# Optimization experiments

Measured on AMD Instinct MI355X. Metric: run time of the kernel, lower is better.

The kernel has to match this reference:

```python
import jax, jax.numpy as jnp
import numpy as np

N_NODES = 100000
N_EDGES = 1600000
IN_F = 512
OUT_F = 128


def setup_inputs() -> dict:
    key = jax.random.key(0)
    k1, k2, k3, k4, k5 = jax.random.split(key, 5)
    features = jax.random.normal(k1, (N_NODES, IN_F), dtype=jnp.float32)
    # xavier_uniform-like init for the [in, out] weight
    limit = float(np.sqrt(6.0 / (IN_F + OUT_F)))
    weight = jax.random.uniform(k2, (IN_F, OUT_F), dtype=jnp.float32, minval=-limit, maxval=limit)
    edge_src = jax.random.randint(k3, (N_EDGES,), 0, N_NODES, dtype=jnp.int32)
    edge_dst = jax.random.randint(k4, (N_EDGES,), 0, N_NODES, dtype=jnp.int32)
    edge_w = jax.random.uniform(k5, (N_EDGES,), dtype=jnp.float32)
    return {"features": features, "weight": weight, "edge_src": edge_src,
            "edge_dst": edge_dst, "edge_w": edge_w}


def reference(features, weight, edge_src, edge_dst, edge_w):
    # support = features @ W  (dense GEMM, [N, out])
    support = features @ weight
    # spmm(adj, support): adj in COO form -> gather source rows, scale by
    # edge weight, scatter-add into destination rows.
    msgs = support[edge_src] * edge_w[:, None]            # [E, out]
    out = jax.ops.segment_sum(msgs, edge_dst, num_segments=N_NODES)  # [N, out]
    return jax.nn.relu(out)
```

## Files before the change

### kernel.cpp

```cpp
#include <hip/hip_runtime.h>
#include <hip/hip_bf16.h>

#define M_N 100000
#define K_F 512
#define N_F 128
#define N_E 1600000
#define NBUK 782
#define CAP 2560
#define EPB 8192

typedef __attribute__((ext_vector_type(8))) short bf16x8;
typedef __attribute__((ext_vector_type(4))) float f32x4;

__device__ __forceinline__ unsigned short f2bf(float f) {
  unsigned u = __float_as_uint(f);
  u += 0x7FFFu + ((u >> 16) & 1u);
  return (unsigned short)(u >> 16);
}

__device__ __forceinline__ unsigned pkbf(float a, float b) {
  __hip_bfloat162 h = __float22bfloat162_rn(make_float2(a, b));
  return *(unsigned*)&h;
}

__global__ void k_wt(const float* __restrict__ w, unsigned short* __restrict__ wtb,
                     int* __restrict__ gcur) {
  int idx = blockIdx.x * 256 + threadIdx.x;
  if (idx < NBUK) gcur[idx] = idx * CAP;
  int k = idx >> 7, n = idx & 127;
  wtb[n * K_F + k] = f2bf(w[idx]);
}

__global__ __launch_bounds__(256, 2) void k_gemm(const float* __restrict__ A,
                       const unsigned short* __restrict__ Bt,
                       unsigned short* __restrict__ S) {
  __shared__ __align__(16) float As[3][128 * 32];
  __shared__ __align__(16) unsigned short Bs[3][128 * 32];
  const int tid = threadIdx.x;
  const int lane = tid & 63;
  const int wv = tid >> 6;
  const int lr = lane & 15, lq = lane >> 4;
  const int bm0 = blockIdx.x * 128;
  const int wrow = wv * 32;

  f32x4 acc[2][8] = {};

#define STAGE(T, BUF)                                                          \
  do {                                                                         \
    _Pragma("unroll") for (int i = 0; i < 4; i++) {                            \
      int idx = i * 256 + tid;                                                 \
      int r = idx >> 3, c = idx & 7;                                           \
      int gr = bm0 + r; if (gr > M_N - 1) gr = M_N - 1;                        \
      const float* srcp = A + (size_t)gr * K_F + (T) * 32 + (c ^ (r & 7)) * 4; \
      __builtin_amdgcn_global_load_lds(                                        \
          (const __attribute__((address_space(1))) void*)srcp,                 \
          (__attribute__((address_space(3))) void*)&As[BUF][(i * 256 + wv * 64) * 4], \
          16, 0, 0);                                                           \
    }                                                                          \
    _Pragma("unroll") for (int i = 0; i < 2; i++) {                            \
      int idx = i * 256 + tid;                                                 \
      int n = idx >> 2, c = idx & 3;                                           \
      const unsigned short* srcb = Bt + (size_t)n * K_F + (T) * 32 + (c ^ (n & 3)) * 8; \
      __builtin_amdgcn_global_load_lds(                                        \
          (const __attribute__((address_space(1))) void*)srcb,                 \
          (__attribute__((address_space(3))) void*)&Bs[BUF][(i * 256 + wv * 64) * 8], \
          16, 0, 0);                                                           \
    }                                                                          \
  } while (0)

  STAGE(0, 0);
  STAGE(1, 1);

#pragma unroll
  for (int t = 0; t < 16; t++) {
    if (t < 15) asm volatile("s_waitcnt vmcnt(6)" ::: "memory");
    else        asm volatile("s_waitcnt vmcnt(0)" ::: "memory");
    __builtin_amdgcn_sched_barrier(0);
    __builtin_amdgcn_s_barrier();
    __builtin_amdgcn_sched_barrier(0);
    if (t < 14) {
      switch ((t + 2) % 3) {
        case 0: STAGE(t + 2, 0); break;
        case 1: STAGE(t + 2, 1); break;
        default: STAGE(t + 2, 2); break;
      }
    }
    const int cb_ = t % 3;
    bf16x8 pb[8];
#pragma unroll
    for (int n = 0; n < 8; n++) {
      int r = n * 16 + lr;
      int cc = lq ^ (r & 3);
      pb[n] = *(const bf16x8*)&Bs[cb_][r * 32 + cc * 8];
    }
#pragma unroll
    for (int m = 0; m < 2; m++) {
      int R = wrow + m * 16 + lr;
      int cb = lq * 2, sw = R & 7;
      f32x4 f0 = *(const f32x4*)&As[cb_][R * 32 + ((cb) ^ sw) * 4];
      f32x4 f1 = *(const f32x4*)&As[cb_][R * 32 + ((cb + 1) ^ sw) * 4];
      uint4 u;
      u.x = pkbf(f0[0], f0[1]);
      u.y = pkbf(f0[2], f0[3]);
      u.z = pkbf(f1[0], f1[1]);
      u.w = pkbf(f1[2], f1[3]);
      bf16x8 af = *(bf16x8*)&u;
#pragma unroll
      for (int n = 0; n < 8; n++)
        acc[m][n] = __builtin_amdgcn_mfma_f32_16x16x32_bf16(af, pb[n], acc[m][n], 0, 0, 0);
    }
  }
#undef STAGE

#pragma unroll
  for (int m = 0; m < 2; m++)
#pragma unroll
    for (int j = 0; j < 4; j++) {
      int gr = bm0 + wrow + m * 16 + lq * 4 + j;
      if (gr < M_N) {
#pragma unroll
        for (int n = 0; n < 8; n++)
          S[(size_t)gr * N_F + n * 16 + lr] = f2bf(acc[m][n][j]);
      }
    }
}

__global__ __launch_bounds__(512) void k_bin(const int* __restrict__ src,
                                             const int* __restrict__ dst,
                                             const float* __restrict__ w,
                                             int* __restrict__ gcur,
                                             uint2* __restrict__ ebin) {
  __shared__ int lh[NBUK];
  __shared__ int lb[NBUK];
  const int tid = threadIdx.x;
  const int e0 = blockIdx.x * EPB;
  for (int b = tid; b < NBUK; b += 512) lh[b] = 0;
  __syncthreads();
#pragma unroll
  for (int i = 0; i < EPB / 512; i++) {
    int e = e0 + i * 512 + tid;
    if (e < N_E) atomicAdd(&lh[dst[e] >> 7], 1);
  }
  __syncthreads();
  for (int b = tid; b < NBUK; b += 512) {
    int c = lh[b];
    lb[b] = c ? atomicAdd(&gcur[b], c) : 0;
    lh[b] = 0;
  }
  __syncthreads();
#pragma unroll
  for (int i = 0; i < EPB / 512; i++) {
    int e = e0 + i * 512 + tid;
    if (e < N_E) {
      int d = dst[e];
      int bk = d >> 7;
      int rank = atomicAdd(&lh[bk], 1);
      ebin[lb[bk] + rank] =
          make_uint2(((unsigned)(d & 127) << 17) | (unsigned)src[e],
                     __float_as_uint(w[e]));
    }
  }
}

__device__ __forceinline__ void fma8(float* acc, float wgt, uint4 v) {
  acc[0] = fmaf(wgt, __uint_as_float(v.x << 16), acc[0]);
  acc[1] = fmaf(wgt, __uint_as_float(v.x & 0xFFFF0000u), acc[1]);
  acc[2] = fmaf(wgt, __uint_as_float(v.y << 16), acc[2]);
  acc[3] = fmaf(wgt, __uint_as_float(v.y & 0xFFFF0000u), acc[3]);
  acc[4] = fmaf(wgt, __uint_as_float(v.z << 16), acc[4]);
  acc[5] = fmaf(wgt, __uint_as_float(v.z & 0xFFFF0000u), acc[5]);
  acc[6] = fmaf(wgt, __uint_as_float(v.w << 16), acc[6]);
  acc[7] = fmaf(wgt, __uint_as_float(v.w & 0xFFFF0000u), acc[7]);
}

__global__ __launch_bounds__(512) void k_bspmm(const unsigned short* __restrict__ S,
                                               const int* __restrict__ gcur,
                                               const uint2* __restrict__ ebin,
                                               float* __restrict__ out) {
  __shared__ uint2 srt[CAP];
  __shared__ int hist[128], excl[129], cur[128];
  const int b = blockIdx.x;
  const int t = threadIdx.x;
  const int cnt = gcur[b] - b * CAP;
  const uint2* eb = ebin + (size_t)b * CAP;

  if (t < 128) hist[t] = 0;
  __syncthreads();

  uint2 er[5];
  int have = 0;
#pragma unroll
  for (int j = 0; j < 5; j++) {
    int i = j * 512 + t;
    if (i < cnt) { er[j] = eb[i]; have = j + 1; }
  }
#pragma unroll
  for (int j = 0; j < 5; j++)
    if (j < have) atomicAdd(&hist[(er[j].x >> 17) & 127], 1);
  __syncthreads();

  if (t < 128) excl[t + 1] = hist[t];
  if (t == 0) excl[0] = 0;
  __syncthreads();
  for (int off = 1; off < 128; off <<= 1) {
    int v = 0;
    if (t < 128) {
      v = excl[t + 1];
      if (t + 1 > off) v += excl[t + 1 - off];
    }
    __syncthreads();
    if (t < 128) excl[t + 1] = v;
    __syncthreads();
  }
  if (t < 128) cur[t] = excl[t];
  __syncthreads();

#pragma unroll
  for (int j = 0; j < 5; j++)
    if (j < have) {
      int dl = (er[j].x >> 17) & 127;
      int r = atomicAdd(&cur[dl], 1);
      srt[r] = er[j];
    }
  __syncthreads();

  const int lane = t & 63, wv = t >> 6;
  const int g = lane >> 4;
  const int l = lane & 15;
  for (int nn = 0; nn < 16; nn++) {
    const int ln = wv * 16 + nn;
    const int s = excl[ln], e = excl[ln + 1];
    float acc[8] = {0.f, 0.f, 0.f, 0.f, 0.f, 0.f, 0.f, 0.f};
    int i = s + g;
    for (; i + 4 < e; i += 8) {
      uint2 p0 = srt[i];
      uint2 p1 = srt[i + 4];
      uint4 v0 = *(const uint4*)(S + (size_t)(p0.x & 0x1FFFFu) * N_F + l * 8);
      uint4 v1 = *(const uint4*)(S + (size_t)(p1.x & 0x1FFFFu) * N_F + l * 8);
      fma8(acc, __uint_as_float(p0.y), v0);
      fma8(acc, __uint_as_float(p1.y), v1);
    }
    if (i < e) {
      uint2 p = srt[i];
      uint4 v = *(const uint4*)(S + (size_t)(p.x & 0x1FFFFu) * N_F + l * 8);
      fma8(acc, __uint_as_float(p.y), v);
    }
#pragma unroll
    for (int j = 0; j < 8; j++) {
      acc[j] += __shfl_xor(acc[j], 16, 64);
      acc[j] += __shfl_xor(acc[j], 32, 64);
      acc[j] = fmaxf(acc[j], 0.f);
    }
    const int node = b * 128 + ln;
    if (g < 2 && node < M_N) {
      float4 r = make_float4(acc[g * 4 + 0], acc[g * 4 + 1],
                             acc[g * 4 + 2], acc[g * 4 + 3]);
      *(float4*)(out + (size_t)node * N_F + l * 8 + g * 4) = r;
    }
  }
}

extern "C" void kernel_launch(void* const* d_in, const int* in_sizes, int n_in,
                              void* d_out, int out_size, void* d_ws, size_t ws_size,
                              hipStream_t stream) {
  const float* features = (const float*)d_in[0];
  const float* weight   = (const float*)d_in[1];
  const int* edge_src   = (const int*)d_in[2];
  const int* edge_dst   = (const int*)d_in[3];
  const float* edge_w   = (const float*)d_in[4];
  float* out = (float*)d_out;

  char* ws = (char*)d_ws;
  size_t off = 0;
  unsigned short* support = (unsigned short*)(ws + off); off += (size_t)M_N * N_F * 2;
  unsigned short* wtb     = (unsigned short*)(ws + off); off += (size_t)N_F * K_F * 2;
  int* gcur   = (int*)(ws + off); off += 4096;
  uint2* ebin = (uint2*)(ws + off); off += ((size_t)NBUK * CAP + 64) * 8;

  k_wt<<<256, 256, 0, stream>>>(weight, wtb, gcur);
  k_gemm<<<(M_N + 127) / 128, 256, 0, stream>>>(features, wtb, support);
  k_bin<<<(N_E + EPB - 1) / EPB, 512, 0, stream>>>(edge_src, edge_dst, edge_w, gcur, ebin);
  k_bspmm<<<NBUK, 512, 0, stream>>>(support, gcur, ebin, out);
}
```

Baseline: 170.2 us.

## Merge GEMM and edge-binning kernels into one launch with block-role split

Folds the edge binning kernel into the GEMM kernel: the first 782 blocks compute the dense GEMM tile and the remaining blocks perform the per-bucket histogram and scatter of edges, reusing the GEMM's shared memory for the histograms. This is meant to overlap the memory-bound binning with the GEMM and remove one kernel launch and its tail. In exchange, binning blocks now run with 256 threads instead of 512 and inherit the GEMM's large shared-memory footprint and launch bounds, which may limit their occupancy.

```diff
diff --git a/kernel.cpp b/kernel.cpp
--- a/kernel.cpp
+++ b/kernel.cpp
@@ -8,6 +8,8 @@
 #define NBUK 782
 #define CAP 2560
 #define EPB 8192
+#define NGEMM 782
+#define NBIN ((N_E + EPB - 1) / EPB)
 
 typedef __attribute__((ext_vector_type(8))) short bf16x8;
 typedef __attribute__((ext_vector_type(4))) float f32x4;
@@ -31,19 +33,24 @@
   wtb[n * K_F + k] = f2bf(w[idx]);
 }
 
-__global__ __launch_bounds__(256, 2) void k_gemm(const float* __restrict__ A,
+__global__ __launch_bounds__(256, 2) void k_fused(const float* __restrict__ A,
                        const unsigned short* __restrict__ Bt,
-                       unsigned short* __restrict__ S) {
+                       unsigned short* __restrict__ S,
+                       const int* __restrict__ esrc, const int* __restrict__ edst,
+                       const float* __restrict__ ew,
+                       int* __restrict__ gcur, uint2* __restrict__ ebin) {
   __shared__ __align__(16) float As[3][128 * 32];
   __shared__ __align__(16) unsigned short Bs[3][128 * 32];
   const int tid = threadIdx.x;
-  const int lane = tid & 63;
-  const int wv = tid >> 6;
-  const int lr = lane & 15, lq = lane >> 4;
-  const int bm0 = blockIdx.x * 128;
-  const int wrow = wv * 32;
-
-  f32x4 acc[2][8] = {};
+
+  if (blockIdx.x < NGEMM) {
+    const int lane = tid & 63;
+    const int wv = tid >> 6;
+    const int lr = lane & 15, lq = lane >> 4;
+    const int bm0 = blockIdx.x * 128;
+    const int wrow = wv * 32;
+
+    f32x4 acc[2][8] = {};
 
 #define STAGE(T, BUF)                                                          \
   do {                                                                         \
@@ -68,96 +75,90 @@
     }                                                                          \
   } while (0)
 
-  STAGE(0, 0);
-  STAGE(1, 1);
-
-#pragma unroll
-  for (int t = 0; t < 16; t++) {
-    if (t < 15) asm volatile("s_waitcnt vmcnt(6)" ::: "memory");
-    else        asm volatile("s_waitcnt vmcnt(0)" ::: "memory");
-    __builtin_amdgcn_sched_barrier(0);
-    __builtin_amdgcn_s_barrier();
-    __builtin_amdgcn_sched_barrier(0);
-    if (t < 14) {
-      switch ((t + 2) % 3) {
-        case 0: STAGE(t + 2, 0); break;
-        case 1: STAGE(t + 2, 1); break;
-        default: STAGE(t + 2, 2); break;
-      }
-    }
-    const int cb_ = t % 3;
-    bf16x8 pb[8];
-#pragma unroll
-    for (int n = 0; n < 8; n++) {
-      int r = n * 16 + lr;
-      int cc = lq ^ (r & 3);
-      pb[n] = *(const bf16x8*)&Bs[cb_][r * 32 + cc * 8];
-    }
-#pragma unroll
-    for (int m = 0; m < 2; m++) {
-      int R = wrow + m * 16 + lr;
-      int cb = lq * 2, sw = R & 7;
-      f32x4 f0 = *(const f32x4*)&As[cb_][R * 32 + ((cb) ^ sw) * 4];
-      f32x4 f1 = *(const f32x4*)&As[cb_][R * 32 + ((cb + 1) ^ sw) * 4];
-      uint4 u;
-      u.x = pkbf(f0[0], f0[1]);
-      u.y = pkbf(f0[2], f0[3]);
-      u.z = pkbf(f1[0], f1[1]);
-      u.w = pkbf(f1[2], f1[3]);
-      bf16x8 af = *(bf16x8*)&u;
-#pragma unroll
-      for (int n = 0; n < 8; n++)
-        acc[m][n] = __builtin_amdgcn_mfma_f32_16x16x32_bf16(af, pb[n], acc[m][n], 0, 0, 0);
-    }
-  }
+    STAGE(0, 0);
+    STAGE(1, 1);
+
+#pragma unroll
+    for (int t = 0; t < 16; t++) {
+      if (t < 15) asm volatile("s_waitcnt vmcnt(6)" ::: "memory");
+      else        asm volatile("s_waitcnt vmcnt(0)" ::: "memory");
+      __builtin_amdgcn_sched_barrier(0);
+      __builtin_amdgcn_s_barrier();
+      __builtin_amdgcn_sched_barrier(0);
+      if (t < 14) {
+        switch ((t + 2) % 3) {
+          case 0: STAGE(t + 2, 0); break;
+          case 1: STAGE(t + 2, 1); break;
+          default: STAGE(t + 2, 2); break;
+        }
+      }
+      const int cb_ = t % 3;
+      bf16x8 pb[8];
+#pragma unroll
+      for (int n = 0; n < 8; n++) {
+        int r = n * 16 + lr;
+        int cc = lq ^ (r & 3);
+        pb[n] = *(const bf16x8*)&Bs[cb_][r * 32 + cc * 8];
+      }
+#pragma unroll
+      for (int m = 0; m < 2; m++) {
+        int R = wrow + m * 16 + lr;
+        int cb = lq * 2, sw = R & 7;
+        f32x4 f0 = *(const f32x4*)&As[cb_][R * 32 + ((cb) ^ sw) * 4];
+        f32x4 f1 = *(const f32x4*)&As[cb_][R * 32 + ((cb + 1) ^ sw) * 4];
+        uint4 u;
+        u.x = pkbf(f0[0], f0[1]);
+        u.y = pkbf(f0[2], f0[3]);
+        u.z = pkbf(f1[0], f1[1]);
+        u.w = pkbf(f1[2], f1[3]);
+        bf16x8 af = *(bf16x8*)&u;
+#pragma unroll
+        for (int n = 0; n < 8; n++)
+          acc[m][n] = __builtin_amdgcn_mfma_f32_16x16x32_bf16(af, pb[n], acc[m][n], 0, 0, 0);
+      }
+    }
 #undef STAGE
 
 #pragma unroll
-  for (int m = 0; m < 2; m++)
-#pragma unroll
-    for (int j = 0; j < 4; j++) {
-      int gr = bm0 + wrow + m * 16 + lq * 4 + j;
-      if (gr < M_N) {
-#pragma unroll
-        for (int n = 0; n < 8; n++)
-          S[(size_t)gr * N_F + n * 16 + lr] = f2bf(acc[m][n][j]);
-      }
-    }
-}
-
-__global__ __launch_bounds__(512) void k_bin(const int* __restrict__ src,
-                                             const int* __restrict__ dst,
-                                             const float* __restrict__ w,
-                                             int* __restrict__ gcur,
-                                             uint2* __restrict__ ebin) {
-  __shared__ int lh[NBUK];
-  __shared__ int lb[NBUK];
-  const int tid = threadIdx.x;
-  const int e0 = blockIdx.x * EPB;
-  for (int b = tid; b < NBUK; b += 512) lh[b] = 0;
-  __syncthreads();
-#pragma unroll
-  for (int i = 0; i < EPB / 512; i++) {
-    int e = e0 + i * 512 + tid;
-    if (e < N_E) atomicAdd(&lh[dst[e] >> 7], 1);
-  }
-  __syncthreads();
-  for (int b = tid; b < NBUK; b += 512) {
-    int c = lh[b];
-    lb[b] = c ? atomicAdd(&gcur[b], c) : 0;
-    lh[b] = 0;
-  }
-  __syncthreads();
-#pragma unroll
-  for (int i = 0; i < EPB / 512; i++) {
-    int e = e0 + i * 512 + tid;
-    if (e < N_E) {
-      int d = dst[e];
-      int bk = d >> 7;
-      int rank = atomicAdd(&lh[bk], 1);
-      ebin[lb[bk] + rank] =
-          make_uint2(((unsigned)(d & 127) << 17) | (unsigned)src[e],
-                     __float_as_uint(w[e]));
+    for (int m = 0; m < 2; m++)
+#pragma unroll
+      for (int j = 0; j < 4; j++) {
+        int gr = bm0 + wrow + m * 16 + lq * 4 + j;
+        if (gr < M_N) {
+#pragma unroll
+          for (int n = 0; n < 8; n++)
+            S[(size_t)gr * N_F + n * 16 + lr] = f2bf(acc[m][n][j]);
+        }
+      }
+  } else {
+    int* lh = (int*)&As[0][0];
+    int* lb = lh + NBUK;
+    const int e0 = (blockIdx.x - NGEMM) * EPB;
+    for (int b = tid; b < NBUK; b += 256) lh[b] = 0;
+    __syncthreads();
+#pragma unroll 4
+    for (int i = 0; i < EPB / 256; i++) {
+      int e = e0 + i * 256 + tid;
+      if (e < N_E) atomicAdd(&lh[edst[e] >> 7], 1);
+    }
+    __syncthreads();
+    for (int b = tid; b < NBUK; b += 256) {
+      int c = lh[b];
+      lb[b] = c ? atomicAdd(&gcur[b], c) : 0;
+      lh[b] = 0;
+    }
+    __syncthreads();
+#pragma unroll 4
+    for (int i = 0; i < EPB / 256; i++) {
+      int e = e0 + i * 256 + tid;
+      if (e < N_E) {
+        int d = edst[e];
+        int bk = d >> 7;
+        int rank = atomicAdd(&lh[bk], 1);
+        ebin[lb[bk] + rank] =
+            make_uint2(((unsigned)(d & 127) << 17) | (unsigned)esrc[e],
+                       __float_as_uint(ew[e]));
+      }
     }
   }
 }
@@ -278,7 +279,7 @@
   uint2* ebin = (uint2*)(ws + off); off += ((size_t)NBUK * CAP + 64) * 8;
 
   k_wt<<<256, 256, 0, stream>>>(weight, wtb, gcur);
-  k_gemm<<<(M_N + 127) / 128, 256, 0, stream>>>(features, wtb, support);
-  k_bin<<<(N_E + EPB - 1) / EPB, 512, 0, stream>>>(edge_src, edge_dst, edge_w, gcur, ebin);
+  k_fused<<<NGEMM + NBIN, 256, 0, stream>>>(features, wtb, support,
+                                            edge_src, edge_dst, edge_w, gcur, ebin);
   k_bspmm<<<NBUK, 512, 0, stream>>>(support, gcur, ebin, out);
 }
```

After: 170.2 us. About the same (+0.0%).

## Replace LDS-staged GEMM with direct register double-buffered global loads

Applied to the files above, without the earlier changes.

The support GEMM no longer stages A and B tiles through shared memory with async global-to-LDS loads and block barriers. Each wave now loads its 32x64 fragment straight into registers with a two-slot register prefetch. The block tile shrinks to 64 rows by splitting the 128 output columns across wave pairs, and occupancy is raised to 3 blocks per CU. This removes LDS traffic and barriers but duplicates A loads across column-halves and relies on L2/cache for reuse. The M_N bound check is dropped because 100000 is divisible by 32.

```diff
diff --git a/kernel.cpp b/kernel.cpp
--- a/kernel.cpp
+++ b/kernel.cpp
@@ -31,97 +31,69 @@
   wtb[n * K_F + k] = f2bf(w[idx]);
 }
 
-__global__ __launch_bounds__(256, 2) void k_gemm(const float* __restrict__ A,
+__global__ __launch_bounds__(256, 3) void k_gemm(const float* __restrict__ A,
                        const unsigned short* __restrict__ Bt,
                        unsigned short* __restrict__ S) {
-  __shared__ __align__(16) float As[3][128 * 32];
-  __shared__ __align__(16) unsigned short Bs[3][128 * 32];
   const int tid = threadIdx.x;
   const int lane = tid & 63;
-  const int wv = tid >> 6;
+  const int w = tid >> 6;
   const int lr = lane & 15, lq = lane >> 4;
-  const int bm0 = blockIdx.x * 128;
-  const int wrow = wv * 32;
-
-  f32x4 acc[2][8] = {};
-
-#define STAGE(T, BUF)                                                          \
-  do {                                                                         \
-    _Pragma("unroll") for (int i = 0; i < 4; i++) {                            \
-      int idx = i * 256 + tid;                                                 \
-      int r = idx >> 3, c = idx & 7;                                           \
-      int gr = bm0 + r; if (gr > M_N - 1) gr = M_N - 1;                        \
-      const float* srcp = A + (size_t)gr * K_F + (T) * 32 + (c ^ (r & 7)) * 4; \
-      __builtin_amdgcn_global_load_lds(                                        \
-          (const __attribute__((address_space(1))) void*)srcp,                 \
-          (__attribute__((address_space(3))) void*)&As[BUF][(i * 256 + wv * 64) * 4], \
-          16, 0, 0);                                                           \
-    }                                                                          \
-    _Pragma("unroll") for (int i = 0; i < 2; i++) {                            \
-      int idx = i * 256 + tid;                                                 \
-      int n = idx >> 2, c = idx & 3;                                           \
-      const unsigned short* srcb = Bt + (size_t)n * K_F + (T) * 32 + (c ^ (n & 3)) * 8; \
-      __builtin_amdgcn_global_load_lds(                                        \
-          (const __attribute__((address_space(1))) void*)srcb,                 \
-          (__attribute__((address_space(3))) void*)&Bs[BUF][(i * 256 + wv * 64) * 8], \
-          16, 0, 0);                                                           \
-    }                                                                          \
-  } while (0)
-
-  STAGE(0, 0);
-  STAGE(1, 1);
-
-#pragma unroll
-  for (int t = 0; t < 16; t++) {
-    if (t < 15) asm volatile("s_waitcnt vmcnt(6)" ::: "memory");
-    else        asm volatile("s_waitcnt vmcnt(0)" ::: "memory");
+  const int row0 = blockIdx.x * 64 + (w & 1) * 32;
+  const int col0 = (w >> 1) * 64;
+  if (row0 >= M_N) return;
+
+  const float* a0 = A + (size_t)(row0 + lr) * K_F + lq * 8;
+  const float* a1 = a0 + (size_t)16 * K_F;
+  const unsigned short* b0 = Bt + (size_t)(col0 + lr) * K_F + lq * 8;
+
+  f32x4 acc[2][4] = {};
+  float4 pa[2][2][2];
+  bf16x8 pb[2][4];
+
+  pa[0][0][0] = *(const float4*)(a0 + 0);
+  pa[0][0][1] = *(const float4*)(a0 + 4);
+  pa[0][1][0] = *(const float4*)(a1 + 0);
+  pa[0][1][1] = *(const float4*)(a1 + 4);
+#pragma unroll
+  for (int n = 0; n < 4; n++)
+    pb[0][n] = *(const bf16x8*)(b0 + (size_t)n * 16 * K_F);
+
+#pragma unroll
+  for (int ks = 0; ks < 16; ks++) {
+    const int cur = ks & 1, nxt = cur ^ 1;
+    if (ks < 15) {
+      const int ko = (ks + 1) * 32;
+      pa[nxt][0][0] = *(const float4*)(a0 + ko);
+      pa[nxt][0][1] = *(const float4*)(a0 + ko + 4);
+      pa[nxt][1][0] = *(const float4*)(a1 + ko);
+      pa[nxt][1][1] = *(const float4*)(a1 + ko + 4);
+#pragma unroll
+      for (int n = 0; n < 4; n++)
+        pb[nxt][n] = *(const bf16x8*)(b0 + (size_t)n * 16 * K_F + ko);
+    }
     __builtin_amdgcn_sched_barrier(0);
-    __builtin_amdgcn_s_barrier();
-    __builtin_amdgcn_sched_barrier(0);
-    if (t < 14) {
-      switch ((t + 2) % 3) {
-        case 0: STAGE(t + 2, 0); break;
-        case 1: STAGE(t + 2, 1); break;
-        default: STAGE(t + 2, 2); break;
-      }
-    }
-    const int cb_ = t % 3;
-    bf16x8 pb[8];
-#pragma unroll
-    for (int n = 0; n < 8; n++) {
-      int r = n * 16 + lr;
-      int cc = lq ^ (r & 3);
-      pb[n] = *(const bf16x8*)&Bs[cb_][r * 32 + cc * 8];
-    }
 #pragma unroll
     for (int m = 0; m < 2; m++) {
-      int R = wrow + m * 16 + lr;
-      int cb = lq * 2, sw = R & 7;
-      f32x4 f0 = *(const f32x4*)&As[cb_][R * 32 + ((cb) ^ sw) * 4];
-      f32x4 f1 = *(const f32x4*)&As[cb_][R * 32 + ((cb + 1) ^ sw) * 4];
       uint4 u;
-      u.x = pkbf(f0[0], f0[1]);
-      u.y = pkbf(f0[2], f0[3]);
-      u.z = pkbf(f1[0], f1[1]);
-      u.w = pkbf(f1[2], f1[3]);
+      u.x = pkbf(pa[cur][m][0].x, pa[cur][m][0].y);
+      u.y = pkbf(pa[cur][m][0].z, pa[cur][m][0].w);
+      u.z = pkbf(pa[cur][m][1].x, pa[cur][m][1].y);
+      u.w = pkbf(pa[cur][m][1].z, pa[cur][m][1].w);
       bf16x8 af = *(bf16x8*)&u;
 #pragma unroll
-      for (int n = 0; n < 8; n++)
-        acc[m][n] = __builtin_amdgcn_mfma_f32_16x16x32_bf16(af, pb[n], acc[m][n], 0, 0, 0);
-    }
-  }
-#undef STAGE
+      for (int n = 0; n < 4; n++)
+        acc[m][n] = __builtin_amdgcn_mfma_f32_16x16x32_bf16(af, pb[cur][n], acc[m][n], 0, 0, 0);
+    }
+  }
 
 #pragma unroll
   for (int m = 0; m < 2; m++)
 #pragma unroll
     for (int j = 0; j < 4; j++) {
-      int gr = bm0 + wrow + m * 16 + lq * 4 + j;
-      if (gr < M_N) {
-#pragma unroll
-        for (int n = 0; n < 8; n++)
-          S[(size_t)gr * N_F + n * 16 + lr] = f2bf(acc[m][n][j]);
-      }
+      int gr = row0 + m * 16 + lq * 4 + j;
+#pragma unroll
+      for (int n = 0; n < 4; n++)
+        S[(size_t)gr * N_F + col0 + n * 16 + lr] = f2bf(acc[m][n][j]);
     }
 }
 
@@ -278,7 +250,7 @@
   uint2* ebin = (uint2*)(ws + off); off += ((size_t)NBUK * CAP + 64) * 8;
 
   k_wt<<<256, 256, 0, stream>>>(weight, wtb, gcur);
-  k_gemm<<<(M_N + 127) / 128, 256, 0, stream>>>(features, wtb, support);
+  k_gemm<<<(M_N + 63) / 64, 256, 0, stream>>>(features, wtb, support);
   k_bin<<<(N_E + EPB - 1) / EPB, 512, 0, stream>>>(edge_src, edge_dst, edge_w, gcur, ebin);
   k_bspmm<<<NBUK, 512, 0, stream>>>(support, gcur, ebin, out);
 }
```

Measured after the change: 232.7 us. 36.8% more time.
